# Kernel optimization log

Measured on AMD Instinct MI355X. Metric: run time of the kernel, lower is better.

## Reference

```python
import jax, jax.numpy as jnp
import numpy as np

SEQ = 4096
D_IN = 1024
D_OUT = 1024


def setup_inputs() -> dict:
    key = jax.random.key(0)
    k1, k2, k3, k4 = jax.random.split(key, 4)
    # Linear weights stored torch-style: [out_features, in_features], scaled for sane magnitudes
    scale = 1.0 / np.sqrt(D_IN)
    return {
        "x": jax.random.normal(k1, (SEQ, D_IN), dtype=jnp.float32),
        "Wq": jax.random.normal(k2, (D_OUT, D_IN), dtype=jnp.float32) * scale,
        "Wk": jax.random.normal(k3, (D_OUT, D_IN), dtype=jnp.float32) * scale,
        "Wv": jax.random.normal(k4, (D_OUT, D_IN), dtype=jnp.float32) * scale,
    }


def reference(x, Wq, Wk, Wv):
    # x: [S, d_in]; W*: [d_out, d_in] (torch nn.Linear layout, no bias)
    q = x @ Wq.T  # [S, d_out]
    k = x @ Wk.T
    v = x @ Wv.T
    d_out = k.shape[-1]
    scores = (q @ k.T) * (1.0 / jnp.sqrt(jnp.float32(d_out)))  # [S, S]
    seq = x.shape[0]
    causal = jnp.tril(jnp.ones((seq, seq), dtype=bool))
    scores = jnp.where(causal, scores, -jnp.inf)
    attn = jax.nn.softmax(scores, axis=-1)
    # dropout(p=0.5) omitted: eval-mode / deterministic baseline
    return attn @ v  # [S, d_out]
```

## Files before the change

kernel.cpp:

```cpp
#include <hip/hip_runtime.h>
#include <hip/hip_bf16.h>
#include <stdint.h>

#define SEQ 4096
#define DIN 1024
#define DOUT 1024

typedef __bf16 bf16;
typedef __bf16 bf16x4v __attribute__((ext_vector_type(4)));
typedef __bf16 bf16x8v __attribute__((ext_vector_type(8)));
typedef float f32x4 __attribute__((ext_vector_type(4)));

#define AS1 __attribute__((address_space(1)))
#define AS3 __attribute__((address_space(3)))

__device__ __forceinline__ void load_lds16(const void* g, void* l) {
  __builtin_amdgcn_global_load_lds((const AS1 uint32_t*)g, (AS3 uint32_t*)l, 16, 0, 0);
}
__device__ __forceinline__ int imin(int a, int b) { return a < b ? a : b; }

__device__ __forceinline__ int xcd_swz(int orig, int nwg) {
  const int q = nwg >> 3, r = nwg & 7;
  const int x = orig & 7, idx = orig >> 3;
  return (x < r ? x * (q + 1) : r * (q + 1) + (x - r) * q) + idx;
}

__global__ __launch_bounds__(256) void cast_all_kernel(
    const float* __restrict__ x, const float* __restrict__ wq,
    const float* __restrict__ wk, const float* __restrict__ wv,
    bf16* __restrict__ xb, bf16* __restrict__ wqb,
    bf16* __restrict__ wkb, bf16* __restrict__ wvb) {
  const int id = blockIdx.x;
  const float* in; bf16* out; int blk;
  if (id < 4096) {
    in = x; out = xb; blk = id;
  } else {
    const int w = (id - 4096) >> 10;
    blk = (id - 4096) & 1023;
    in = (w == 0) ? wq : (w == 1) ? wk : wv;
    out = (w == 0) ? wqb : (w == 1) ? wkb : wvb;
  }
  const int i = (blk * 256 + threadIdx.x) * 4;
  float4 v = *reinterpret_cast<const float4*>(in + i);
  bf16x4v o;
  o[0] = (bf16)v.x; o[1] = (bf16)v.y; o[2] = (bf16)v.z; o[3] = (bf16)v.w;
  *reinterpret_cast<bf16x4v*>(out + i) = o;
}

struct G256 {
  const char *pa, *pb;
  size_t lda2, ldb2;
  char* lds;
  int tid;
};

__device__ __forceinline__ void stage_tile(const G256& g, int sd, int kt) {
  const size_t kb = (size_t)kt * 128;
  char* d = g.lds + sd * 65536;
  const int to = g.tid * 16;
  load_lds16(g.pa + kb,                  d + 0     + to);
  load_lds16(g.pa + kb + 64  * g.lda2,   d + 8192  + to);
  load_lds16(g.pb + kb,                  d + 32768 + to);
  load_lds16(g.pb + kb + 64  * g.ldb2,   d + 40960 + to);
  load_lds16(g.pb + kb + 128 * g.ldb2,   d + 49152 + to);
  load_lds16(g.pb + kb + 192 * g.ldb2,   d + 57344 + to);
  load_lds16(g.pa + kb + 128 * g.lda2,   d + 16384 + to);
  load_lds16(g.pa + kb + 192 * g.lda2,   d + 24576 + to);
}

__device__ __forceinline__ void gemm256_core(const bf16* __restrict__ A,
                                             const bf16* __restrict__ B,
                                             int lda, int ldb, int brow, int bcol,
                                             int kt0, int ktn,
                                             f32x4 acc[2][2][4][2], char* lds) {
  const int tid = threadIdx.x;
  const int sr = tid >> 3;
  const int cs = ((tid & 7) << 4) ^ ((sr & 7) << 4);
  G256 g;
  g.lda2 = (size_t)lda * 2; g.ldb2 = (size_t)ldb * 2;
  g.pa = (const char*)A + (size_t)(brow + sr) * g.lda2 + cs;
  g.pb = (const char*)B + (size_t)(bcol + sr) * g.ldb2 + cs;
  g.lds = lds; g.tid = tid;

  const int lane = tid & 63, lrow = lane & 15, lkg = lane >> 4;
  const int wave = tid >> 6, wm = wave >> 2, wn = wave & 3;
  const int aReg = wm * 16384;
  const int bReg = 32768 + (wn >> 1) * 16384;
  const int brow0 = (wn & 1) * 64;
  const int swz = (lrow & 7) << 4;

  stage_tile(g, 0, kt0);
  asm volatile("s_waitcnt vmcnt(0)" ::: "memory");
  __builtin_amdgcn_s_barrier();
  __builtin_amdgcn_sched_barrier(0);

  for (int t = 0; t < ktn; ++t) {
    const int d = t & 1;
    stage_tile(g, d ^ 1, kt0 + imin(t + 1, ktn - 1));
    const char* db = lds + d * 65536;

    bf16x8v a[4][2], b0[2][2], b1[2][2];
#pragma unroll
    for (int nt = 0; nt < 2; ++nt)
#pragma unroll
      for (int ks = 0; ks < 2; ++ks) {
        const int ck = (ks * 64 + lkg * 16) ^ swz;
        b0[nt][ks] = *(const bf16x8v*)(db + bReg + (brow0 + nt * 16 + lrow) * 128 + ck);
        b1[nt][ks] = *(const bf16x8v*)(db + bReg + (brow0 + 32 + nt * 16 + lrow) * 128 + ck);
      }
#pragma unroll
    for (int mt = 0; mt < 4; ++mt)
#pragma unroll
      for (int ks = 0; ks < 2; ++ks)
        a[mt][ks] = *(const bf16x8v*)(db + aReg + (mt * 16 + lrow) * 128 + ((ks * 64 + lkg * 16) ^ swz));
    __builtin_amdgcn_s_setprio(1);
#pragma unroll
    for (int mt = 0; mt < 4; ++mt)
#pragma unroll
      for (int nt = 0; nt < 2; ++nt)
#pragma unroll
        for (int ks = 0; ks < 2; ++ks) {
          acc[0][0][mt][nt] = __builtin_amdgcn_mfma_f32_16x16x32_bf16(a[mt][ks], b0[nt][ks], acc[0][0][mt][nt], 0, 0, 0);
          acc[0][1][mt][nt] = __builtin_amdgcn_mfma_f32_16x16x32_bf16(a[mt][ks], b1[nt][ks], acc[0][1][mt][nt], 0, 0, 0);
        }
    __builtin_amdgcn_s_setprio(0);
#pragma unroll
    for (int mt = 0; mt < 4; ++mt)
#pragma unroll
      for (int ks = 0; ks < 2; ++ks)
        a[mt][ks] = *(const bf16x8v*)(db + aReg + ((64 + mt * 16 + lrow) * 128) + ((ks * 64 + lkg * 16) ^ swz));
    __builtin_amdgcn_s_setprio(1);
#pragma unroll
    for (int mt = 0; mt < 4; ++mt)
#pragma unroll
      for (int nt = 0; nt < 2; ++nt)
#pragma unroll
        for (int ks = 0; ks < 2; ++ks) {
          acc[1][1][mt][nt] = __builtin_amdgcn_mfma_f32_16x16x32_bf16(a[mt][ks], b1[nt][ks], acc[1][1][mt][nt], 0, 0, 0);
          acc[1][0][mt][nt] = __builtin_amdgcn_mfma_f32_16x16x32_bf16(a[mt][ks], b0[nt][ks], acc[1][0][mt][nt], 0, 0, 0);
        }
    __builtin_amdgcn_s_setprio(0);
    asm volatile("s_waitcnt vmcnt(0)" ::: "memory");
    __builtin_amdgcn_s_barrier();
    __builtin_amdgcn_sched_barrier(0);
  }
}

struct G128 {
  const char *pa, *pb;
  size_t lda2, ldb2;
  char* lds;
  int tid;
};

__device__ __forceinline__ void stage_tile128(const G128& g, int sd, int kt) {
  const size_t kb = (size_t)kt * 128;
  char* d = g.lds + sd * 49152;
  const int to = g.tid * 16;
  load_lds16(g.pa + kb,                 d + 0     + to);
  load_lds16(g.pa + kb + 64 * g.lda2,   d + 8192  + to);
  load_lds16(g.pb + kb,                 d + 16384 + to);
  load_lds16(g.pb + kb + 64  * g.ldb2,  d + 24576 + to);
  load_lds16(g.pb + kb + 128 * g.ldb2,  d + 32768 + to);
  load_lds16(g.pb + kb + 192 * g.ldb2,  d + 40960 + to);
}

__device__ __forceinline__ void gemm128_core(const bf16* __restrict__ A,
                                             const bf16* __restrict__ B,
                                             int lda, int ldb, int brow, int bcol,
                                             int kt0, int ktn,
                                             f32x4 acc[2][4][2], char* lds) {
  const int tid = threadIdx.x;
  const int sr = tid >> 3;
  const int cs = ((tid & 7) << 4) ^ ((sr & 7) << 4);
  G128 g;
  g.lda2 = (size_t)lda * 2; g.ldb2 = (size_t)ldb * 2;
  g.pa = (const char*)A + (size_t)(brow + sr) * g.lda2 + cs;
  g.pb = (const char*)B + (size_t)(bcol + sr) * g.ldb2 + cs;
  g.lds = lds; g.tid = tid;

  const int lane = tid & 63, lrow = lane & 15, lkg = lane >> 4;
  const int wave = tid >> 6, wm = wave >> 2, wn = wave & 3;
  const int swz = (lrow & 7) << 4;

  stage_tile128(g, 0, kt0);
  asm volatile("s_waitcnt vmcnt(0)" ::: "memory");
  __builtin_amdgcn_s_barrier();
  __builtin_amdgcn_sched_barrier(0);

  for (int t = 0; t < ktn; ++t) {
    const int d = t & 1;
    stage_tile128(g, d ^ 1, kt0 + imin(t + 1, ktn - 1));
    const char* db = lds + d * 49152;

    bf16x8v a[4][2], b0[2][2], b1[2][2];
#pragma unroll
    for (int nt = 0; nt < 2; ++nt)
#pragma unroll
      for (int ks = 0; ks < 2; ++ks) {
        const int ck = (ks * 64 + lkg * 16) ^ swz;
        b0[nt][ks] = *(const bf16x8v*)(db + 16384 + (wn * 64 + nt * 16 + lrow) * 128 + ck);
        b1[nt][ks] = *(const bf16x8v*)(db + 16384 + (wn * 64 + 32 + nt * 16 + lrow) * 128 + ck);
      }
#pragma unroll
    for (int mt = 0; mt < 4; ++mt)
#pragma unroll
      for (int ks = 0; ks < 2; ++ks)
        a[mt][ks] = *(const bf16x8v*)(db + (wm * 64 + mt * 16 + lrow) * 128 + ((ks * 64 + lkg * 16) ^ swz));
    __builtin_amdgcn_s_setprio(1);
#pragma unroll
    for (int mt = 0; mt < 4; ++mt)
#pragma unroll
      for (int nt = 0; nt < 2; ++nt)
#pragma unroll
        for (int ks = 0; ks < 2; ++ks) {
          acc[0][mt][nt] = __builtin_amdgcn_mfma_f32_16x16x32_bf16(a[mt][ks], b0[nt][ks], acc[0][mt][nt], 0, 0, 0);
          acc[1][mt][nt] = __builtin_amdgcn_mfma_f32_16x16x32_bf16(a[mt][ks], b1[nt][ks], acc[1][mt][nt], 0, 0, 0);
        }
    __builtin_amdgcn_s_setprio(0);
    asm volatile("s_waitcnt vmcnt(0)" ::: "memory");
    __builtin_amdgcn_s_barrier();
    __builtin_amdgcn_sched_barrier(0);
  }
}

#define ACC256_INIT()                         \
  f32x4 acc[2][2][4][2];                      \
  {                                           \
    f32x4 z = {0.f, 0.f, 0.f, 0.f};           \
    for (int a1 = 0; a1 < 2; ++a1)            \
      for (int a2 = 0; a2 < 2; ++a2)          \
        for (int a3 = 0; a3 < 4; ++a3)        \
          for (int a4 = 0; a4 < 2; ++a4) acc[a1][a2][a3][a4] = z; \
  }

#define EPI_BASES()                                             \
  const int lane = threadIdx.x & 63;                            \
  const int wave = threadIdx.x >> 6;                            \
  const int wm = wave >> 2, wn = wave & 3;                      \
  const int rb = wm * 128 + ((lane >> 4) << 2);                 \
  const int cb = wn * 64 + (lane & 15);

__global__ __launch_bounds__(512, 2) void qk_kernel(const bf16* __restrict__ xb,
                                                    const bf16* __restrict__ Wq,
                                                    const bf16* __restrict__ Wk,
                                                    bf16* __restrict__ Q,
                                                    bf16* __restrict__ K) {
  extern __shared__ char lds[];
  const int l = xcd_swz(blockIdx.x, 256);
  const int z = l >> 7, tt = l & 127, bi = tt >> 2, bj = tt & 3;
  const bf16* W = (z == 0) ? Wq : Wk;
  f32x4 acc[2][4][2];
  {
    f32x4 zr = {0.f, 0.f, 0.f, 0.f};
    for (int a1 = 0; a1 < 2; ++a1)
      for (int a2 = 0; a2 < 4; ++a2)
        for (int a3 = 0; a3 < 2; ++a3) acc[a1][a2][a3] = zr;
  }
  gemm128_core(xb, W, DIN, DIN, bi * 128, bj * 256, 0, 16, acc, lds);
  const int lane = threadIdx.x & 63;
  const int wave = threadIdx.x >> 6;
  const int wm = wave >> 2, wn = wave & 3;
  const int rbase = bi * 128 + wm * 64 + ((lane >> 4) << 2);
  const int cbase = bj * 256 + wn * 64 + (lane & 15);
  bf16* O = (z == 0) ? Q : K;
#pragma unroll
  for (int nh = 0; nh < 2; ++nh)
#pragma unroll
    for (int mt = 0; mt < 4; ++mt)
#pragma unroll
      for (int nt = 0; nt < 2; ++nt)
#pragma unroll
        for (int j = 0; j < 4; ++j)
          O[(size_t)(rbase + mt * 16 + j) * DOUT + (cbase + nh * 32 + nt * 16)] =
              (bf16)acc[nh][mt][nt][j];
}

__global__ __launch_bounds__(512, 2) void scores_v_kernel(const bf16* __restrict__ Q,
                                                          const bf16* __restrict__ Km,
                                                          bf16* __restrict__ Scb,
                                                          const bf16* __restrict__ xb,
                                                          const bf16* __restrict__ Wv,
                                                          bf16* __restrict__ Vt) {
  extern __shared__ char lds[];
  const int l = xcd_swz(blockIdx.x, 200);
  if (l < 64) {
    const int bi = l >> 2, bj = l & 3;
    ACC256_INIT();
    gemm256_core(xb, Wv, DIN, DIN, bi * 256, bj * 256, 0, 16, acc, lds);
    EPI_BASES();
    const int rbase = bi * 256 + rb, cbase = bj * 256 + cb;
#pragma unroll
    for (int mh = 0; mh < 2; ++mh)
#pragma unroll
      for (int nh = 0; nh < 2; ++nh)
#pragma unroll
        for (int mt = 0; mt < 4; ++mt)
#pragma unroll
          for (int nt = 0; nt < 2; ++nt)
#pragma unroll
            for (int j = 0; j < 4; ++j)
              Vt[(size_t)(cbase + nh * 32 + nt * 16) * SEQ + (rbase + mh * 64 + mt * 16 + j)] =
                  (bf16)acc[mh][nh][mt][nt][j];
  } else {
    const int t = l - 64;
    int bi = (int)((sqrtf(8.0f * (float)t + 1.0f) - 1.0f) * 0.5f);
    while ((bi + 1) * (bi + 2) / 2 <= t) ++bi;
    while (bi * (bi + 1) / 2 > t) --bi;
    const int bj = t - bi * (bi + 1) / 2;
    ACC256_INIT();
    gemm256_core(Q, Km, DOUT, DOUT, bi * 256, bj * 256, 0, 16, acc, lds);
    EPI_BASES();
    const int rbase = bi * 256 + rb, cbase = bj * 256 + cb;
    const float scale = 0.03125f;
#pragma unroll
    for (int mh = 0; mh < 2; ++mh)
#pragma unroll
      for (int nh = 0; nh < 2; ++nh)
#pragma unroll
        for (int mt = 0; mt < 4; ++mt)
#pragma unroll
          for (int nt = 0; nt < 2; ++nt)
#pragma unroll
            for (int j = 0; j < 4; ++j)
              Scb[(size_t)(rbase + mh * 64 + mt * 16 + j) * SEQ + (cbase + nh * 32 + nt * 16)] =
                  (bf16)(acc[mh][nh][mt][nt][j] * scale);
  }
}

__global__ __launch_bounds__(256) void softmax_kernel(const bf16* __restrict__ Scb,
                                                      bf16* __restrict__ P) {
  __shared__ float rowbuf[SEQ];
  __shared__ float red[8];
  const int r = (SEQ - 1) - blockIdx.x;
  const int n = r + 1;
  const int nw8 = ((r >> 8) + 1) << 5;
  const int tid = threadIdx.x;
  const bf16* src = Scb + (size_t)r * SEQ;
  const float NEG = -__builtin_inff();

  float lmax = NEG;
  for (int g = tid; g < nw8; g += 256) {
    bf16x8v v = *reinterpret_cast<const bf16x8v*>(src + g * 8);
    const int b = g * 8;
    float f[8];
#pragma unroll
    for (int j = 0; j < 8; ++j) {
      f[j] = (b + j < n) ? (float)v[j] : NEG;
      lmax = fmaxf(lmax, f[j]);
    }
    reinterpret_cast<float4*>(rowbuf)[g * 2]     = make_float4(f[0], f[1], f[2], f[3]);
    reinterpret_cast<float4*>(rowbuf)[g * 2 + 1] = make_float4(f[4], f[5], f[6], f[7]);
  }
#pragma unroll
  for (int m = 32; m >= 1; m >>= 1) lmax = fmaxf(lmax, __shfl_xor(lmax, m, 64));
  if ((tid & 63) == 0) red[tid >> 6] = lmax;
  __syncthreads();
  const float rmax = fmaxf(fmaxf(red[0], red[1]), fmaxf(red[2], red[3]));

  const int nw4 = nw8 * 2;
  float lsum = 0.f;
  for (int g = tid; g < nw4; g += 256) {
    float4 v = reinterpret_cast<const float4*>(rowbuf)[g];
    v.x = __expf(v.x - rmax);
    v.y = __expf(v.y - rmax);
    v.z = __expf(v.z - rmax);
    v.w = __expf(v.w - rmax);
    reinterpret_cast<float4*>(rowbuf)[g] = v;
    lsum += v.x + v.y + v.z + v.w;
  }
#pragma unroll
  for (int m = 32; m >= 1; m >>= 1) lsum += __shfl_xor(lsum, m, 64);
  if ((tid & 63) == 0) red[4 + (tid >> 6)] = lsum;
  __syncthreads();
  const float inv = 1.0f / (red[4] + red[5] + red[6] + red[7]);

  bf16* dst = P + (size_t)r * SEQ;
  for (int g = tid; g < nw4; g += 256) {
    float4 v = reinterpret_cast<const float4*>(rowbuf)[g];
    bf16x4v o;
    o[0] = (bf16)(v.x * inv);
    o[1] = (bf16)(v.y * inv);
    o[2] = (bf16)(v.z * inv);
    o[3] = (bf16)(v.w * inv);
    *reinterpret_cast<bf16x4v*>(dst + g * 4) = o;
  }
}

__device__ __constant__ int kPref[13] = {0, 1, 2, 3, 5, 7, 9, 12, 15, 18, 22, 26, 30};

__device__ __forceinline__ float* par_slot(float* p0, float* p1, int slot) {
  return (slot < 128) ? p0 + (size_t)slot * 65536
                      : p1 + (size_t)(slot - 128) * 65536;
}

__global__ __launch_bounds__(512, 2) void pv_kernel(const bf16* __restrict__ P,
                                                    const bf16* __restrict__ Vt,
                                                    float* __restrict__ Out,
                                                    float* __restrict__ Par0,
                                                    float* __restrict__ Par1) {
  extern __shared__ char lds[];
  const int l = xcd_swz(blockIdx.x, 204);
  const int bj = l & 3;
  int c = l >> 2, bi = 0;
  for (;;) {
    const int nch = (bi + 3) / 3;
    if (c < nch) break;
    c -= nch; ++bi;
  }
  const int nch = (bi + 3) / 3;
  const int Ti = (bi + 1) * 4;
  const int base = Ti / nch, rem = Ti % nch;
  const int kt0 = c * base + imin(c, rem);
  const int ktn = base + (c < rem ? 1 : 0);
  ACC256_INIT();
  gemm256_core(P, Vt, SEQ, SEQ, bi * 256, bj * 256, kt0, ktn, acc, lds);
  EPI_BASES();
  if (c == nch - 1) {
    const int rbase = bi * 256 + rb, cbase = bj * 256 + cb;
#pragma unroll
    for (int mh = 0; mh < 2; ++mh)
#pragma unroll
      for (int nh = 0; nh < 2; ++nh)
#pragma unroll
        for (int mt = 0; mt < 4; ++mt)
#pragma unroll
          for (int nt = 0; nt < 2; ++nt)
#pragma unroll
            for (int j = 0; j < 4; ++j)
              Out[(size_t)(rbase + mh * 64 + mt * 16 + j) * DOUT + (cbase + nh * 32 + nt * 16)] =
                  acc[mh][nh][mt][nt][j];
  } else {
    const int slot = (kPref[bi - 3] + c) * 4 + bj;
    float* Pp = par_slot(Par0, Par1, slot);
#pragma unroll
    for (int mh = 0; mh < 2; ++mh)
#pragma unroll
      for (int nh = 0; nh < 2; ++nh)
#pragma unroll
        for (int mt = 0; mt < 4; ++mt)
#pragma unroll
          for (int nt = 0; nt < 2; ++nt)
#pragma unroll
            for (int j = 0; j < 4; ++j)
              Pp[(rb + mh * 64 + mt * 16 + j) * 256 + (cb + nh * 32 + nt * 16)] =
                  acc[mh][nh][mt][nt][j];
  }
}

__global__ __launch_bounds__(256) void reduce_kernel(float* __restrict__ Par0,
                                                     float* __restrict__ Par1,
                                                     float* __restrict__ Out) {
  const int blk = blockIdx.x;
  const int t2 = blk >> 6, sub = blk & 63;
  const int bi = 3 + (t2 >> 2), bj = t2 & 3;
  const int npart = (bi + 3) / 3 - 1;
  const int pb = kPref[bi - 3] * 4 + bj;
  const int elem = sub * 1024 + threadIdx.x * 4;
  const int r = elem >> 8, cc = elem & 255;
  float* op = Out + (size_t)(bi * 256 + r) * DOUT + bj * 256 + cc;
  float4 o = *reinterpret_cast<float4*>(op);
  for (int p = 0; p < npart; ++p) {
    const float* Pp = par_slot(Par0, Par1, pb + p * 4);
    const float4 v = *reinterpret_cast<const float4*>(Pp + elem);
    o.x += v.x; o.y += v.y; o.z += v.z; o.w += v.w;
  }
  *reinterpret_cast<float4*>(op) = o;
}

extern "C" void kernel_launch(void* const* d_in, const int* in_sizes, int n_in,
                              void* d_out, int out_size, void* d_ws, size_t ws_size,
                              hipStream_t stream) {
  const float* x  = (const float*)d_in[0];
  const float* Wq = (const float*)d_in[1];
  const float* Wk = (const float*)d_in[2];
  const float* Wv = (const float*)d_in[3];
  float* Out = (float*)d_out;

  char* base = (char*)d_ws;
  bf16* xb   = (bf16*)(base + 0);
  bf16* wqb  = (bf16*)(base + 8388608);
  bf16* wkb  = (bf16*)(base + 10485760);
  bf16* wvb  = (bf16*)(base + 12582912);
  bf16* Qb   = (bf16*)(base + 14680064);
  bf16* Kb   = (bf16*)(base + 23068672);
  bf16* Vtb  = (bf16*)(base + 31457280);
  bf16* Scb  = (bf16*)(base + 39845888);
  float* Par0 = (float*)(base + 73400320);
  float* Par1 = (float*)(base + 0);
  bf16* P    = (bf16*)(base + 106954752);

  (void)hipFuncSetAttribute((const void*)qk_kernel,
                            hipFuncAttributeMaxDynamicSharedMemorySize, 98304);
  (void)hipFuncSetAttribute((const void*)scores_v_kernel,
                            hipFuncAttributeMaxDynamicSharedMemorySize, 131072);
  (void)hipFuncSetAttribute((const void*)pv_kernel,
                            hipFuncAttributeMaxDynamicSharedMemorySize, 131072);

  cast_all_kernel<<<7168, 256, 0, stream>>>(x, Wq, Wk, Wv, xb, wqb, wkb, wvb);

  qk_kernel<<<256, 512, 98304, stream>>>(xb, wqb, wkb, Qb, Kb);
  scores_v_kernel<<<200, 512, 131072, stream>>>(Qb, Kb, Scb, xb, wvb, Vtb);
  softmax_kernel<<<SEQ, 256, 0, stream>>>(Scb, P);
  pv_kernel<<<204, 512, 131072, stream>>>(P, Vtb, Out, Par0, Par1);
  reduce_kernel<<<3328, 256, 0, stream>>>(Par0, Par1, Out);
}
```

Baseline: 111.6 us.

## Interleave tile staging with MFMA phases and triple-buffer the 128 GEMM

The 256-tile GEMM core now issues the next tile's global-to-LDS loads in pairs between its four MFMA quadrant phases and waits with partial vmcnt counts instead of draining all loads at the end of each iteration. The 128-tile core moves to a three-stage LDS ring with a prefetch distance of two tiles and one barrier per iteration, so qk_kernel's dynamic LDS grows to 144 KB. The goal is to hide global load latency behind matrix math and cut full-drain stalls. The risks are extra barriers in the 256 path, correctness depending on precise vmcnt ordering, and higher LDS use per block.

```diff
diff --git a/kernel.cpp b/kernel.cpp
--- a/kernel.cpp
+++ b/kernel.cpp
@@ -17,6 +17,7 @@
 __device__ __forceinline__ void load_lds16(const void* g, void* l) {
   __builtin_amdgcn_global_load_lds((const AS1 uint32_t*)g, (AS3 uint32_t*)l, 16, 0, 0);
 }
+
 __device__ __forceinline__ int imin(int a, int b) { return a < b ? a : b; }
 
 __device__ __forceinline__ int xcd_swz(int orig, int nwg) {
@@ -54,19 +55,10 @@
   int tid;
 };
 
-__device__ __forceinline__ void stage_tile(const G256& g, int sd, int kt) {
-  const size_t kb = (size_t)kt * 128;
-  char* d = g.lds + sd * 65536;
-  const int to = g.tid * 16;
-  load_lds16(g.pa + kb,                  d + 0     + to);
-  load_lds16(g.pa + kb + 64  * g.lda2,   d + 8192  + to);
-  load_lds16(g.pb + kb,                  d + 32768 + to);
-  load_lds16(g.pb + kb + 64  * g.ldb2,   d + 40960 + to);
-  load_lds16(g.pb + kb + 128 * g.ldb2,   d + 49152 + to);
-  load_lds16(g.pb + kb + 192 * g.ldb2,   d + 57344 + to);
-  load_lds16(g.pa + kb + 128 * g.lda2,   d + 16384 + to);
-  load_lds16(g.pa + kb + 192 * g.lda2,   d + 24576 + to);
-}
+#define STG256(sd_, kt_, ldsOff_, rowOff_, isA_)                              \
+  load_lds16(((isA_) ? g.pa : g.pb) + (size_t)(kt_) * 128 +                   \
+                 (size_t)(rowOff_) * ((isA_) ? g.lda2 : g.ldb2),              \
+             g.lds + (sd_) * 65536 + (ldsOff_) + g.tid * 16)
 
 __device__ __forceinline__ void gemm256_core(const bf16* __restrict__ A,
                                              const bf16* __restrict__ B,
@@ -89,59 +81,96 @@
   const int brow0 = (wn & 1) * 64;
   const int swz = (lrow & 7) << 4;
 
-  stage_tile(g, 0, kt0);
-  asm volatile("s_waitcnt vmcnt(0)" ::: "memory");
-  __builtin_amdgcn_s_barrier();
-  __builtin_amdgcn_sched_barrier(0);
+  STG256(0, kt0, 0,     0,   1);
+  STG256(0, kt0, 16384, 128, 1);
+  STG256(0, kt0, 32768, 0,   0);
+  STG256(0, kt0, 40960, 64,  0);
+  STG256(0, kt0, 49152, 128, 0);
+  STG256(0, kt0, 57344, 192, 0);
+  STG256(0, kt0, 8192,  64,  1);
+  STG256(0, kt0, 24576, 192, 1);
 
   for (int t = 0; t < ktn; ++t) {
-    const int d = t & 1;
-    stage_tile(g, d ^ 1, kt0 + imin(t + 1, ktn - 1));
+    const int d = t & 1, sd = d ^ 1;
     const char* db = lds + d * 65536;
-
-    bf16x8v a[4][2], b0[2][2], b1[2][2];
+    const int kn = kt0 + imin(t + 1, ktn - 1);
+
+    asm volatile("s_waitcnt vmcnt(2)" ::: "memory");
+    __builtin_amdgcn_s_barrier();
+    __builtin_amdgcn_sched_barrier(0);
+
+    bf16x8v a0[4][2], a1[4][2], b0[2][2], b1[2][2];
+#pragma unroll
+    for (int mt = 0; mt < 4; ++mt)
+#pragma unroll
+      for (int ks = 0; ks < 2; ++ks)
+        a0[mt][ks] = *(const bf16x8v*)(db + aReg + (mt * 16 + lrow) * 128 + ((ks * 64 + lkg * 16) ^ swz));
 #pragma unroll
     for (int nt = 0; nt < 2; ++nt)
 #pragma unroll
-      for (int ks = 0; ks < 2; ++ks) {
-        const int ck = (ks * 64 + lkg * 16) ^ swz;
-        b0[nt][ks] = *(const bf16x8v*)(db + bReg + (brow0 + nt * 16 + lrow) * 128 + ck);
-        b1[nt][ks] = *(const bf16x8v*)(db + bReg + (brow0 + 32 + nt * 16 + lrow) * 128 + ck);
-      }
-#pragma unroll
-    for (int mt = 0; mt < 4; ++mt)
-#pragma unroll
       for (int ks = 0; ks < 2; ++ks)
-        a[mt][ks] = *(const bf16x8v*)(db + aReg + (mt * 16 + lrow) * 128 + ((ks * 64 + lkg * 16) ^ swz));
+        b0[nt][ks] = *(const bf16x8v*)(db + bReg + (brow0 + nt * 16 + lrow) * 128 + ((ks * 64 + lkg * 16) ^ swz));
+    STG256(sd, kn, 0,     0,   1);
+    STG256(sd, kn, 16384, 128, 1);
     __builtin_amdgcn_s_setprio(1);
 #pragma unroll
     for (int mt = 0; mt < 4; ++mt)
 #pragma unroll
       for (int nt = 0; nt < 2; ++nt)
 #pragma unroll
-        for (int ks = 0; ks < 2; ++ks) {
-          acc[0][0][mt][nt] = __builtin_amdgcn_mfma_f32_16x16x32_bf16(a[mt][ks], b0[nt][ks], acc[0][0][mt][nt], 0, 0, 0);
-          acc[0][1][mt][nt] = __builtin_amdgcn_mfma_f32_16x16x32_bf16(a[mt][ks], b1[nt][ks], acc[0][1][mt][nt], 0, 0, 0);
-        }
+        for (int ks = 0; ks < 2; ++ks)
+          acc[0][0][mt][nt] = __builtin_amdgcn_mfma_f32_16x16x32_bf16(a0[mt][ks], b0[nt][ks], acc[0][0][mt][nt], 0, 0, 0);
     __builtin_amdgcn_s_setprio(0);
-#pragma unroll
-    for (int mt = 0; mt < 4; ++mt)
+
+#pragma unroll
+    for (int nt = 0; nt < 2; ++nt)
 #pragma unroll
       for (int ks = 0; ks < 2; ++ks)
-        a[mt][ks] = *(const bf16x8v*)(db + aReg + ((64 + mt * 16 + lrow) * 128) + ((ks * 64 + lkg * 16) ^ swz));
+        b1[nt][ks] = *(const bf16x8v*)(db + bReg + (brow0 + 32 + nt * 16 + lrow) * 128 + ((ks * 64 + lkg * 16) ^ swz));
+    STG256(sd, kn, 32768, 0,  0);
+    STG256(sd, kn, 40960, 64, 0);
     __builtin_amdgcn_s_setprio(1);
 #pragma unroll
     for (int mt = 0; mt < 4; ++mt)
 #pragma unroll
       for (int nt = 0; nt < 2; ++nt)
 #pragma unroll
-        for (int ks = 0; ks < 2; ++ks) {
-          acc[1][1][mt][nt] = __builtin_amdgcn_mfma_f32_16x16x32_bf16(a[mt][ks], b1[nt][ks], acc[1][1][mt][nt], 0, 0, 0);
-          acc[1][0][mt][nt] = __builtin_amdgcn_mfma_f32_16x16x32_bf16(a[mt][ks], b0[nt][ks], acc[1][0][mt][nt], 0, 0, 0);
-        }
+        for (int ks = 0; ks < 2; ++ks)
+          acc[0][1][mt][nt] = __builtin_amdgcn_mfma_f32_16x16x32_bf16(a0[mt][ks], b1[nt][ks], acc[0][1][mt][nt], 0, 0, 0);
     __builtin_amdgcn_s_setprio(0);
-    asm volatile("s_waitcnt vmcnt(0)" ::: "memory");
+
+    asm volatile("s_waitcnt vmcnt(4)" ::: "memory");
     __builtin_amdgcn_s_barrier();
+    __builtin_amdgcn_sched_barrier(0);
+
+#pragma unroll
+    for (int mt = 0; mt < 4; ++mt)
+#pragma unroll
+      for (int ks = 0; ks < 2; ++ks)
+        a1[mt][ks] = *(const bf16x8v*)(db + aReg + ((64 + mt * 16 + lrow) * 128) + ((ks * 64 + lkg * 16) ^ swz));
+    STG256(sd, kn, 49152, 128, 0);
+    STG256(sd, kn, 57344, 192, 0);
+    __builtin_amdgcn_s_setprio(1);
+#pragma unroll
+    for (int mt = 0; mt < 4; ++mt)
+#pragma unroll
+      for (int nt = 0; nt < 2; ++nt)
+#pragma unroll
+        for (int ks = 0; ks < 2; ++ks)
+          acc[1][1][mt][nt] = __builtin_amdgcn_mfma_f32_16x16x32_bf16(a1[mt][ks], b1[nt][ks], acc[1][1][mt][nt], 0, 0, 0);
+    __builtin_amdgcn_s_setprio(0);
+
+    STG256(sd, kn, 8192,  64,  1);
+    STG256(sd, kn, 24576, 192, 1);
+    __builtin_amdgcn_s_setprio(1);
+#pragma unroll
+    for (int mt = 0; mt < 4; ++mt)
+#pragma unroll
+      for (int nt = 0; nt < 2; ++nt)
+#pragma unroll
+        for (int ks = 0; ks < 2; ++ks)
+          acc[1][0][mt][nt] = __builtin_amdgcn_mfma_f32_16x16x32_bf16(a1[mt][ks], b0[nt][ks], acc[1][0][mt][nt], 0, 0, 0);
+    __builtin_amdgcn_s_setprio(0);
     __builtin_amdgcn_sched_barrier(0);
   }
 }
@@ -184,13 +213,16 @@
   const int swz = (lrow & 7) << 4;
 
   stage_tile128(g, 0, kt0);
-  asm volatile("s_waitcnt vmcnt(0)" ::: "memory");
-  __builtin_amdgcn_s_barrier();
-  __builtin_amdgcn_sched_barrier(0);
-
+  stage_tile128(g, 1, kt0 + imin(1, ktn - 1));
+
+  int d = 0;
   for (int t = 0; t < ktn; ++t) {
-    const int d = t & 1;
-    stage_tile128(g, d ^ 1, kt0 + imin(t + 1, ktn - 1));
+    asm volatile("s_waitcnt vmcnt(6)" ::: "memory");
+    __builtin_amdgcn_s_barrier();
+    __builtin_amdgcn_sched_barrier(0);
+
+    int sd = d + 2; if (sd >= 3) sd -= 3;
+    stage_tile128(g, sd, kt0 + imin(t + 2, ktn - 1));
     const char* db = lds + d * 49152;
 
     bf16x8v a[4][2], b0[2][2], b1[2][2];
@@ -218,9 +250,8 @@
           acc[1][mt][nt] = __builtin_amdgcn_mfma_f32_16x16x32_bf16(a[mt][ks], b1[nt][ks], acc[1][mt][nt], 0, 0, 0);
         }
     __builtin_amdgcn_s_setprio(0);
-    asm volatile("s_waitcnt vmcnt(0)" ::: "memory");
-    __builtin_amdgcn_s_barrier();
     __builtin_amdgcn_sched_barrier(0);
+    if (++d == 3) d = 0;
   }
 }
 
@@ -491,7 +522,7 @@
   bf16* P    = (bf16*)(base + 106954752);
 
   (void)hipFuncSetAttribute((const void*)qk_kernel,
-                            hipFuncAttributeMaxDynamicSharedMemorySize, 98304);
+                            hipFuncAttributeMaxDynamicSharedMemorySize, 147456);
   (void)hipFuncSetAttribute((const void*)scores_v_kernel,
                             hipFuncAttributeMaxDynamicSharedMemorySize, 131072);
   (void)hipFuncSetAttribute((const void*)pv_kernel,
@@ -499,7 +530,7 @@
 
   cast_all_kernel<<<7168, 256, 0, stream>>>(x, Wq, Wk, Wv, xb, wqb, wkb, wvb);
 
-  qk_kernel<<<256, 512, 98304, stream>>>(xb, wqb, wkb, Qb, Kb);
+  qk_kernel<<<256, 512, 147456, stream>>>(xb, wqb, wkb, Qb, Kb);
   scores_v_kernel<<<200, 512, 131072, stream>>>(Qb, Kb, Scb, xb, wvb, Vtb);
   softmax_kernel<<<SEQ, 256, 0, stream>>>(Scb, P);
   pv_kernel<<<204, 512, 131072, stream>>>(P, Vtb, Out, Par0, Par1);
```

Measured after the change: 108.5 us. -2.8%, faster.
